# Kernel tuning notes

Hardware: AMD Instinct MI355X
Metric: run time of the kernel (lower is better)

Reference implementation:

```python
import jax, jax.numpy as jnp
import numpy as np

B, C, H, W = 8, 1024, 32, 32   # batch, in_channels (cnn==vit), spatial
OUT = 2048                     # out_channels
NHEAD = 32                     # heads -> head_dim 64
EMBED_DIM = 1024               # used ONLY for the softmax scale (faithful to source)
LN_EPS = 1e-5


def setup_inputs() -> dict:
    key = jax.random.key(0)
    ks = jax.random.split(key, 8)
    f = lambda k, s: jax.random.normal(k, s, dtype=jnp.float32)
    return {
        "x_cnn": f(ks[0], (B, C, H, W)),
        "x_vit": f(ks[1], (B, C, H, W)),
        "Wq": f(ks[2], (OUT, C)) * 0.02, "bq": jnp.zeros((OUT,), jnp.float32),
        "Wk": f(ks[3], (OUT, C)) * 0.02, "bk": jnp.zeros((OUT,), jnp.float32),
        "Wv": f(ks[4], (OUT, C)) * 0.02, "bv": jnp.zeros((OUT,), jnp.float32),
        "w_mix": jnp.float32(0.5),
        "ln_g": jnp.ones((OUT,), jnp.float32), "ln_b": jnp.zeros((OUT,), jnp.float32),
        "Wfc": f(ks[5], (OUT, OUT)) * 0.02, "bfc": jnp.zeros((OUT,), jnp.float32),
    }


def _mha(Q, K, V):
    # Q,K,V: [b, n, OUT] -> multi-head attention, scale by sqrt(EMBED_DIM) as in source
    b, n, _ = Q.shape
    d = OUT // NHEAD
    Qh = Q.reshape(b, n, NHEAD, d)
    Kh = K.reshape(b, n, NHEAD, d)
    Vh = V.reshape(b, n, NHEAD, d)
    scores = jnp.einsum('bqhd,bkhd->bhqk', Qh, Kh) / jnp.sqrt(jnp.float32(EMBED_DIM))
    attn = jax.nn.softmax(scores, axis=-1)
    out = jnp.einsum('bhqk,bkhd->bqhd', attn, Vh)
    return out.reshape(b, n, OUT)


def reference(x_cnn, x_vit, Wq, bq, Wk, bk, Wv, bv, w_mix, ln_g, ln_b, Wfc, bfc):
    b, c, h, w = x_cnn.shape
    xc = x_cnn.reshape(b, c, h * w).transpose(0, 2, 1)   # [b, hw, c]
    xv = x_vit.reshape(b, c, h * w).transpose(0, 2, 1)
    # shared projections, two cross directions
    Q1 = xc @ Wq.T + bq; K1 = xv @ Wk.T + bk; V1 = xv @ Wv.T + bv
    Q2 = xv @ Wq.T + bq; K2 = xc @ Wk.T + bk; V2 = xc @ Wv.T + bv
    attended_vit = _mha(Q1, K1, V1)   # cnn queries attend vit
    attended_cnn = _mha(Q2, K2, V2)   # vit queries attend cnn
    r = attended_cnn * w_mix + attended_vit * (1.0 - w_mix)
    # LayerNorm over last dim (population variance, like torch)
    mu = jnp.mean(r, axis=-1, keepdims=True)
    var = jnp.var(r, axis=-1, keepdims=True)
    r = (r - mu) / jnp.sqrt(var + LN_EPS) * ln_g + ln_b
    r = r @ Wfc.T + bfc
    return r.transpose(0, 2, 1).reshape(b, OUT, h, w)
```

## Files before the change

### kernel.cpp

```cpp
#include <hip/hip_runtime.h>
#include <stdint.h>

typedef unsigned short u16;
typedef unsigned int u32;
typedef __attribute__((ext_vector_type(4))) float float4v;
typedef __attribute__((ext_vector_type(4))) unsigned int uint4v;
typedef __attribute__((ext_vector_type(4))) unsigned short u16x4;
typedef __attribute__((ext_vector_type(8))) short s16x8;
typedef __attribute__((ext_vector_type(4))) float f32x4;

__device__ __forceinline__ float bf2f(u16 h) {
    union { u32 u; float f; } v; v.u = ((u32)h) << 16; return v.f;
}
__device__ __forceinline__ u16 f2bf(float f) {
    union { float f; u32 u; } v; v.f = f;
    return (u16)((v.u + 0x8000u) >> 16);
}
__device__ __forceinline__ float exp2_fast(float x) {
    float r; asm("v_exp_f32 %0, %1" : "=v"(r) : "v"(x)); return r;
}

__device__ __forceinline__ bool detect_f32(const u16* lng) {
    return *(const u32*)lng == 0x3F800000u;
}

__device__ __forceinline__ float read_wmix(const void* wmix) {
    u32 word = *(const u32*)wmix;
    if ((word & 0xFFFFu) == 0u) {
        union { u32 u; float f; } v; v.u = word; return v.f;
    }
    return bf2f((u16)(word & 0xFFFFu));
}

__device__ __forceinline__ uint4v load8(const void* base, long long off, bool isF32) {
    if (isF32) {
        const float* p = (const float*)base + off;
        float4v f0 = *(const float4v*)p;
        float4v f1 = *(const float4v*)(p + 4);
        uint4v r; u16* h = (u16*)&r;
#pragma unroll
        for (int i = 0; i < 4; ++i) { h[i] = f2bf(f0[i]); h[4 + i] = f2bf(f1[i]); }
        return r;
    }
    return *(const uint4v*)((const u16*)base + off);
}
__device__ __forceinline__ float loadraw(const void* p, int idx, bool isF32) {
    return isF32 ? ((const float*)p)[idx] : bf2f(((const u16*)p)[idx]);
}

__global__ __launch_bounds__(256) void convert_w(
    const void* __restrict__ src, u16* __restrict__ dst, int n,
    const u16* __restrict__ lng)
{
    bool f32 = detect_f32(lng);
    long long i = ((long long)blockIdx.x * 256 + threadIdx.x) * 8;
    if (i >= n) return;
    uint4v v = load8(src, i, f32);
    *(uint4v*)(dst + i) = v;
}

__global__ __launch_bounds__(256) void transpose_k(
    const void* __restrict__ xc, const void* __restrict__ xv,
    u16* __restrict__ xt, const u16* __restrict__ lng)
{
    bool f32 = detect_f32(lng);
    int z = blockIdx.z;
    const void* xbase = (z < 8 ? xc : xv);
    long long soff = (long long)(z & 7) * 1024 * 1024;
    u16* outp = xt + (long long)z * 1024 * 1024;
    int c0 = blockIdx.x * 64, p0 = blockIdx.y * 64;
    __shared__ u16 t[64][72];
    int tid = threadIdx.x;
    int cl = tid >> 3, ch = tid & 7;
#pragma unroll
    for (int pass = 0; pass < 2; ++pass) {
        int c = cl + pass * 32;
        uint4v v = load8(xbase, soff + (long long)(c0 + c) * 1024 + p0 + ch * 8, f32);
        const u16* vv = (const u16*)&v;
#pragma unroll
        for (int i = 0; i < 8; ++i) t[ch * 8 + i][c] = vv[i];
    }
    __syncthreads();
#pragma unroll
    for (int pass = 0; pass < 2; ++pass) {
        int p = cl + pass * 32;
        uint4v v; u16* vv = (u16*)&v;
#pragma unroll
        for (int i = 0; i < 8; ++i) vv[i] = t[p][ch * 8 + i];
        *(uint4v*)(outp + (long long)(p0 + p) * 1024 + c0 + ch * 8) = v;
    }
}

__global__ __launch_bounds__(256) void transpose_v(
    const u16* __restrict__ V, u16* __restrict__ VT)
{
    int b = blockIdx.z, head = blockIdx.y, p0 = blockIdx.x * 64;
    const u16* src = V + (long long)b * 1024 * 2048 + head * 64;
    u16* dst = VT + (long long)(b * 32 + head) * 64 * 1024;
    __shared__ u16 t[64][72];
    int tid = threadIdx.x;
    int r = tid >> 3, ch = tid & 7;
#pragma unroll
    for (int pass = 0; pass < 2; ++pass) {
        int p = r + pass * 32;
        uint4v v = *(const uint4v*)(src + (long long)(p0 + p) * 2048 + ch * 8);
        const u16* vv = (const u16*)&v;
#pragma unroll
        for (int i = 0; i < 8; ++i) t[ch * 8 + i][p] = vv[i];
    }
    __syncthreads();
#pragma unroll
    for (int pass = 0; pass < 2; ++pass) {
        int d = r + pass * 32;
        uint4v v = *(const uint4v*)&t[d][ch * 8];
        *(uint4v*)(dst + (long long)d * 1024 + p0 + ch * 8) = v;
    }
}

__global__ __launch_bounds__(256) void gemm_mfma(
    const void* __restrict__ A, int lda, long long sA, int a_raw,
    const void* __restrict__ B, int ldb, long long sB, int b_raw,
    const void* __restrict__ bias,
    void* __restrict__ Cv, int ldc, long long sC, int c_f32,
    int K, int bias_on_m, const u16* __restrict__ lng)
{
    bool f32 = detect_f32(lng);
    bool aF = f32 && a_raw, bF = f32 && b_raw;
    int gx = gridDim.x, gy = gridDim.y, gz = gridDim.z;
    int flat = blockIdx.x + gx * (blockIdx.y + gy * blockIdx.z);
    int nwg = gx * gy * gz;
    int wsw = ((nwg & 7) == 0) ? ((flat & 7) * (nwg >> 3) + (flat >> 3)) : flat;
    int byi = wsw % gy, rem = wsw / gy;
    int bxi = rem % gx, z = rem / gx;

    long long aoff = (long long)z * sA, boff = (long long)z * sB;
    long long coff = (long long)z * sC;
    int m0 = bxi * 128, n0 = byi * 128;
    int tid = threadIdx.x;
    int lane = tid & 63, wave = tid >> 6;
    int lrow = lane & 15, lgrp = lane >> 4;
    int wm = (wave >> 1) * 64, wn = (wave & 1) * 64;

    __shared__ u16 As[128][72];
    __shared__ u16 Bs[128][72];

    f32x4 acc[4][4];
#pragma unroll
    for (int i = 0; i < 4; ++i)
#pragma unroll
        for (int j = 0; j < 4; ++j) acc[i][j] = (f32x4)0.f;

    int sr = tid >> 3;
    int kc = (tid & 7) * 8;

    long long arow[4], brow[4];
#pragma unroll
    for (int q = 0; q < 4; ++q) {
        arow[q] = aoff + (long long)(m0 + sr + q * 32) * lda;
        brow[q] = boff + (long long)(n0 + sr + q * 32) * ldb;
    }

    uint4v an[4], bn[4];
#pragma unroll
    for (int q = 0; q < 4; ++q) {
        an[q] = load8(A, arow[q] + kc, aF);
        bn[q] = load8(B, brow[q] + kc, bF);
    }

    for (int k0 = 0; k0 < K; k0 += 64) {
        uint4v ac[4], bc[4];
#pragma unroll
        for (int q = 0; q < 4; ++q) { ac[q] = an[q]; bc[q] = bn[q]; }
        __syncthreads();
#pragma unroll
        for (int q = 0; q < 4; ++q) {
            *(uint4v*)&As[sr + q * 32][kc] = ac[q];
            *(uint4v*)&Bs[sr + q * 32][kc] = bc[q];
        }
        __syncthreads();
        if (k0 + 64 < K) {
#pragma unroll
            for (int q = 0; q < 4; ++q) {
                an[q] = load8(A, arow[q] + k0 + 64 + kc, aF);
                bn[q] = load8(B, brow[q] + k0 + 64 + kc, bF);
            }
        }
#pragma unroll
        for (int kk = 0; kk < 2; ++kk) {
            s16x8 af[4], bfr[4];
#pragma unroll
            for (int i = 0; i < 4; ++i)
                af[i] = *(const s16x8*)&As[wm + i * 16 + lrow][kk * 32 + lgrp * 8];
#pragma unroll
            for (int j = 0; j < 4; ++j)
                bfr[j] = *(const s16x8*)&Bs[wn + j * 16 + lrow][kk * 32 + lgrp * 8];
#pragma unroll
            for (int i = 0; i < 4; ++i)
#pragma unroll
                for (int j = 0; j < 4; ++j)
                    acc[i][j] = __builtin_amdgcn_mfma_f32_16x16x32_bf16(
                        af[i], bfr[j], acc[i][j], 0, 0, 0);
        }
    }

    float bnj[4];
#pragma unroll
    for (int j = 0; j < 4; ++j)
        bnj[j] = bias_on_m ? 0.f : loadraw(bias, n0 + wn + j * 16 + lrow, f32);
#pragma unroll
    for (int i = 0; i < 4; ++i) {
#pragma unroll
        for (int e = 0; e < 4; ++e) {
            int mrow = m0 + wm + i * 16 + lgrp * 4 + e;
            float bm = bias_on_m ? loadraw(bias, mrow, f32) : 0.f;
#pragma unroll
            for (int j = 0; j < 4; ++j) {
                int ncol = n0 + wn + j * 16 + lrow;
                float val = acc[i][j][e] + (bias_on_m ? bm : bnj[j]);
                long long idx = coff + (long long)mrow * ldc + ncol;
                if (c_f32) ((float*)Cv)[idx] = val;
                else       ((u16*)Cv)[idx] = f2bf(val);
            }
        }
    }
}

__global__ __launch_bounds__(256) void attn_mfma(
    u16* __restrict__ Qb, const u16* __restrict__ Kb, const u16* __restrict__ VTb)
{
    const int ld = 2048;
    const float SCL = 0.0450985123f;
    int flat = blockIdx.x + 16 * (blockIdx.y + 32 * blockIdx.z);
    int w = (flat & 7) * 512 + (flat >> 3);
    int qt = w & 15, head = (w >> 4) & 31, bz = w >> 9;
    int q0 = qt * 64;
    long long base = (long long)bz * 1024 * ld + head * 64;
    u16* Q = Qb + base;
    const u16* K = Kb + base;
    const u16* VT = VTb + (long long)(bz * 32 + head) * 64 * 1024;

    int tid = threadIdx.x;
    int wave = tid >> 6, lane = tid & 63;
    int lrow = lane & 15, lgrp = lane >> 4;

    __shared__ u16 Kt[64][72];
    __shared__ u16 VTt[64][72];
    __shared__ u16 Pt[4][16][72];

    int qw = q0 + wave * 16;
    s16x8 qf0, qf1;
    {
        const u16* qp = Q + (long long)(qw + lrow) * ld + lgrp * 8;
        qf0 = *(const s16x8*)qp;
        qf1 = *(const s16x8*)(qp + 32);
    }
    s16x8 onesf;
#pragma unroll
    for (int e = 0; e < 8; ++e) ((u16*)&onesf)[e] = 0x3F80;

    f32x4 of[4];
#pragma unroll
    for (int dt = 0; dt < 4; ++dt) of[dt] = (f32x4)0.f;
    f32x4 osum = (f32x4)0.f;
    float mL = 0.f;

    int skey = tid >> 2, sc4 = tid & 3;
    const u16* kptr = K + (long long)skey * ld + sc4 * 8;
    const u16* vptr = VT + (long long)skey * 1024 + sc4 * 16;
    uint4v ka0 = *(const uint4v*)kptr;
    uint4v ka1 = *(const uint4v*)(kptr + 32);
    uint4v va0 = *(const uint4v*)vptr;
    uint4v va1 = *(const uint4v*)(vptr + 8);

    for (int t = 0; t < 16; ++t) {
        *(uint4v*)&Kt[skey][sc4 * 8]       = ka0;
        *(uint4v*)&Kt[skey][sc4 * 8 + 32]  = ka1;
        *(uint4v*)&VTt[skey][sc4 * 16]     = va0;
        *(uint4v*)&VTt[skey][sc4 * 16 + 8] = va1;
        if (t < 15) {
            kptr += 64 * ld;
            vptr += 64;
            ka0 = *(const uint4v*)kptr;
            ka1 = *(const uint4v*)(kptr + 32);
            va0 = *(const uint4v*)vptr;
            va1 = *(const uint4v*)(vptr + 8);
        }
        __syncthreads();

        f32x4 sf[4];
#pragma unroll
        for (int f = 0; f < 4; ++f) {
            s16x8 kf0 = *(const s16x8*)&Kt[f * 16 + lrow][lgrp * 8];
            s16x8 kf1 = *(const s16x8*)&Kt[f * 16 + lrow][lgrp * 8 + 32];
            f32x4 a = (f32x4)0.f;
            a = __builtin_amdgcn_mfma_f32_16x16x32_bf16(kf0, qf0, a, 0, 0, 0);
            a = __builtin_amdgcn_mfma_f32_16x16x32_bf16(kf1, qf1, a, 0, 0, 0);
            sf[f] = a;
        }

        float t0 = fmaxf(fmaxf(sf[0][0], sf[0][1]), sf[0][2]);
        float t1 = fmaxf(fmaxf(sf[0][3], sf[1][0]), sf[1][1]);
        float t2 = fmaxf(fmaxf(sf[1][2], sf[1][3]), sf[2][0]);
        float t3 = fmaxf(fmaxf(sf[2][1], sf[2][2]), sf[2][3]);
        float t4 = fmaxf(fmaxf(sf[3][0], sf[3][1]), sf[3][2]);
        float u0 = fmaxf(fmaxf(t0, t1), t2);
        float u1 = fmaxf(fmaxf(t3, t4), sf[3][3]);
        float mx = fmaxf(u0, u1);
        mx = fmaxf(mx, __shfl_xor(mx, 16));
        mx = fmaxf(mx, __shfl_xor(mx, 32));
        if (__any(mx * SCL > mL + 8.f)) {
            float mLn = fmaxf(mL, mx * SCL);
            float sc = exp2_fast(mL - mLn);
#pragma unroll
            for (int dt = 0; dt < 4; ++dt)
#pragma unroll
                for (int i = 0; i < 4; ++i) of[dt][i] *= sc;
#pragma unroll
            for (int i = 0; i < 4; ++i) osum[i] *= sc;
            mL = mLn;
        }

        float nmL = -mL;
#pragma unroll
        for (int f = 0; f < 4; ++f) {
            float p0 = exp2_fast(fmaf(sf[f][0], SCL, nmL));
            float p1 = exp2_fast(fmaf(sf[f][1], SCL, nmL));
            float p2 = exp2_fast(fmaf(sf[f][2], SCL, nmL));
            float p3 = exp2_fast(fmaf(sf[f][3], SCL, nmL));
            union { u32 w[2]; u16x4 v; } pu;
            asm("v_cvt_pk_bf16_f32 %0, %1, %2" : "=v"(pu.w[0]) : "v"(p0), "v"(p1));
            asm("v_cvt_pk_bf16_f32 %0, %1, %2" : "=v"(pu.w[1]) : "v"(p2), "v"(p3));
            *(u16x4*)&Pt[wave][lrow][f * 16 + lgrp * 4] = pu.v;
        }
        asm volatile("s_waitcnt lgkmcnt(0)" ::: "memory");
        __builtin_amdgcn_sched_barrier(0);

#pragma unroll
        for (int kk = 0; kk < 2; ++kk) {
            s16x8 pb = *(const s16x8*)&Pt[wave][lrow][kk * 32 + lgrp * 8];
            osum = __builtin_amdgcn_mfma_f32_16x16x32_bf16(onesf, pb, osum, 0, 0, 0);
#pragma unroll
            for (int dt = 0; dt < 4; ++dt) {
                s16x8 va = *(const s16x8*)&VTt[dt * 16 + lrow][kk * 32 + lgrp * 8];
                of[dt] = __builtin_amdgcn_mfma_f32_16x16x32_bf16(va, pb, of[dt], 0, 0, 0);
            }
        }
        __syncthreads();
    }

    float linv = 1.f / osum[0];
#pragma unroll
    for (int dt = 0; dt < 4; ++dt) {
        u16x4 o;
#pragma unroll
        for (int i = 0; i < 4; ++i) o[i] = f2bf(of[dt][i] * linv);
        *(u16x4*)(Q + (long long)(qw + lrow) * ld + dt * 16 + lgrp * 4) = o;
    }
}

__global__ __launch_bounds__(256) void mix_ln_k(
    const u16* __restrict__ Avit, const u16* __restrict__ Acnn,
    const void* __restrict__ wmix,
    const void* __restrict__ g, const void* __restrict__ bta,
    u16* __restrict__ Y, const u16* __restrict__ lng)
{
    bool f32 = detect_f32(lng);
    long long row = blockIdx.x;
    const u16* a0 = Avit + row * 2048;
    const u16* a1 = Acnn + row * 2048;
    int tid = threadIdx.x, lane = tid & 63, wave = tid >> 6;
    float w = read_wmix(wmix);
    int o = tid * 8;
    uint4v x0 = *(const uint4v*)(a0 + o);
    uint4v x1 = *(const uint4v*)(a1 + o);
    const u16* p0 = (const u16*)&x0;
    const u16* p1 = (const u16*)&x1;
    float r[8], sum = 0.f, sq = 0.f;
#pragma unroll
    for (int e = 0; e < 8; ++e) {
        r[e] = w * bf2f(p1[e]) + (1.f - w) * bf2f(p0[e]);
        sum += r[e]; sq += r[e] * r[e];
    }
#pragma unroll
    for (int off = 1; off < 64; off <<= 1) {
        sum += __shfl_xor(sum, off);
        sq += __shfl_xor(sq, off);
    }
    __shared__ float red[8];
    if (lane == 0) { red[wave] = sum; red[4 + wave] = sq; }
    __syncthreads();
    sum = red[0] + red[1] + red[2] + red[3];
    sq = red[4] + red[5] + red[6] + red[7];
    float mu = sum * (1.f / 2048.f);
    float var = sq * (1.f / 2048.f) - mu * mu;
    float rstd = rsqrtf(var + 1e-5f);
    uint4v y; u16* py = (u16*)&y;
#pragma unroll
    for (int e = 0; e < 8; ++e)
        py[e] = f2bf((r[e] - mu) * rstd * loadraw(g, o + e, f32) + loadraw(bta, o + e, f32));
    *(uint4v*)(Y + row * 2048 + o) = y;
}

extern "C" void kernel_launch(void* const* d_in, const int* in_sizes, int n_in,
                              void* d_out, int out_size, void* d_ws, size_t ws_size,
                              hipStream_t stream)
{
    const void* x_cnn = d_in[0];
    const void* x_vit = d_in[1];
    const void* Wq = d_in[2];
    const void* bq = d_in[3];
    const void* Wk = d_in[4];
    const void* bk = d_in[5];
    const void* Wv = d_in[6];
    const void* bv = d_in[7];
    const void* wmix = d_in[8];
    const u16* ln_g = (const u16*)d_in[9];
    const void* ln_b = d_in[10];
    const void* Wfc = d_in[11];
    const void* bfc = d_in[12];

    u16* X   = (u16*)d_out;
    u16* VTb = (u16*)((char*)d_out + 33554432);
    char* ws = (char*)d_ws;
    const long long SEG = 33554432LL;
    const long long SRC = 8LL * 1024 * 1024;

    bool fused = ws_size >= (size_t)(6 * SEG + 20971520LL);
    bool tail  = fused || ws_size >= (size_t)(4 * SEG + 20971520LL);
    u16* S[6];
    for (int i = 0; i < 6; ++i) S[i] = (u16*)(ws + i * SEG);
    u16* WqB = (u16*)(ws + (fused ? 6 : 4) * SEG);
    u16* WkB = WqB + 2097152;
    u16* WvB = WkB + 2097152;
    u16* WfB = WvB + 2097152;
    if (tail) {
        convert_w<<<1024, 256, 0, stream>>>(Wq, WqB, 2097152, ln_g);
        convert_w<<<1024, 256, 0, stream>>>(Wk, WkB, 2097152, ln_g);
        convert_w<<<1024, 256, 0, stream>>>(Wv, WvB, 2097152, ln_g);
        convert_w<<<2048, 256, 0, stream>>>(Wfc, WfB, 4194304, ln_g);
    }
    const void* pWq = tail ? (const void*)WqB : Wq;
    const void* pWk = tail ? (const void*)WkB : Wk;
    const void* pWv = tail ? (const void*)WvB : Wv;
    const void* pWf = tail ? (const void*)WfB : Wfc;
    int rawW = tail ? 0 : 1;

    transpose_k<<<dim3(16, 16, 16), 256, 0, stream>>>(x_cnn, x_vit, X, ln_g);

    if (fused) {
        dim3 fg(128, 16, 1);
        gemm_mfma<<<fg, 256, 0, stream>>>(X, 1024, 0LL, 0, pWq, 1024, 0LL, rawW, bq,
                                          S[0], 2048, 0LL, 0, 1024, 0, ln_g);
        gemm_mfma<<<fg, 256, 0, stream>>>(X, 1024, 0LL, 0, pWk, 1024, 0LL, rawW, bk,
                                          S[2], 2048, 0LL, 0, 1024, 0, ln_g);
        gemm_mfma<<<fg, 256, 0, stream>>>(X, 1024, 0LL, 0, pWv, 1024, 0LL, rawW, bv,
                                          S[4], 2048, 0LL, 0, 1024, 0, ln_g);
        transpose_v<<<dim3(16, 32, 8), 256, 0, stream>>>(S[5], VTb);
        attn_mfma<<<dim3(16, 32, 8), 256, 0, stream>>>(S[0], S[3], VTb);
        transpose_v<<<dim3(16, 32, 8), 256, 0, stream>>>(S[4], VTb);
        attn_mfma<<<dim3(16, 32, 8), 256, 0, stream>>>(S[1], S[2], VTb);
        mix_ln_k<<<8192, 256, 0, stream>>>(S[0], S[1], wmix, ln_g, ln_b, S[2], ln_g);
    } else {
        dim3 pg(64, 16, 1);
        gemm_mfma<<<pg, 256, 0, stream>>>(X,       1024, 0LL, 0, pWq, 1024, 0LL, rawW, bq,
                                          S[0], 2048, 0LL, 0, 1024, 0, ln_g);
        gemm_mfma<<<pg, 256, 0, stream>>>(X + SRC, 1024, 0LL, 0, pWk, 1024, 0LL, rawW, bk,
                                          S[1], 2048, 0LL, 0, 1024, 0, ln_g);
        gemm_mfma<<<pg, 256, 0, stream>>>(X + SRC, 1024, 0LL, 0, pWv, 1024, 0LL, rawW, bv,
                                          S[2], 2048, 0LL, 0, 1024, 0, ln_g);
        transpose_v<<<dim3(16, 32, 8), 256, 0, stream>>>(S[2], VTb);
        attn_mfma<<<dim3(16, 32, 8), 256, 0, stream>>>(S[0], S[1], VTb);
        gemm_mfma<<<pg, 256, 0, stream>>>(X + SRC, 1024, 0LL, 0, pWq, 1024, 0LL, rawW, bq,
                                          S[1], 2048, 0LL, 0, 1024, 0, ln_g);
        gemm_mfma<<<pg, 256, 0, stream>>>(X,       1024, 0LL, 0, pWk, 1024, 0LL, rawW, bk,
                                          S[2], 2048, 0LL, 0, 1024, 0, ln_g);
        gemm_mfma<<<pg, 256, 0, stream>>>(X,       1024, 0LL, 0, pWv, 1024, 0LL, rawW, bv,
                                          S[3], 2048, 0LL, 0, 1024, 0, ln_g);
        transpose_v<<<dim3(16, 32, 8), 256, 0, stream>>>(S[3], VTb);
        attn_mfma<<<dim3(16, 32, 8), 256, 0, stream>>>(S[1], S[2], VTb);
        mix_ln_k<<<8192, 256, 0, stream>>>(S[0], S[1], wmix, ln_g, ln_b, S[2], ln_g);
    }

    gemm_mfma<<<dim3(16, 8, 8), 256, 0, stream>>>(pWf, 2048, 0LL, rawW, S[2], 2048, 1024LL * 2048, 0, bfc,
                                                  d_out, 1024, 2048LL * 1024, 1, 2048, 1, ln_g);
}
```

Before: 890.5 us.

## Use direct global-to-LDS loads with swizzle in GEMM and merge attention launches

The bf16 GEMM path now loads tiles straight from global memory into LDS with global_load_lds, using an XOR swizzle to avoid bank conflicts. The register staging and software prefetch are dropped, so loads no longer overlap compute within a K step. The two cross-attention directions are merged into one launch with a doubled grid, using separate VT buffers placed in the output region. The online-softmax max reduction is now only done across the full wave when a rescale is needed.

```diff
diff --git a/kernel.cpp b/kernel.cpp
--- a/kernel.cpp
+++ b/kernel.cpp
@@ -18,6 +18,11 @@
 }
 __device__ __forceinline__ float exp2_fast(float x) {
     float r; asm("v_exp_f32 %0, %1" : "=v"(r) : "v"(x)); return r;
+}
+__device__ __forceinline__ void glds16(const u16* g, u16* l) {
+    __builtin_amdgcn_global_load_lds(
+        (const __attribute__((address_space(1))) u32*)(const void*)g,
+        (__attribute__((address_space(3))) u32*)(void*)l, 16, 0, 0);
 }
 
 __device__ __forceinline__ bool detect_f32(const u16* lng) {
@@ -150,56 +155,97 @@
 #pragma unroll
         for (int j = 0; j < 4; ++j) acc[i][j] = (f32x4)0.f;
 
-    int sr = tid >> 3;
-    int kc = (tid & 7) * 8;
-
-    long long arow[4], brow[4];
-#pragma unroll
-    for (int q = 0; q < 4; ++q) {
-        arow[q] = aoff + (long long)(m0 + sr + q * 32) * lda;
-        brow[q] = boff + (long long)(n0 + sr + q * 32) * ldb;
-    }
-
-    uint4v an[4], bn[4];
-#pragma unroll
-    for (int q = 0; q < 4; ++q) {
-        an[q] = load8(A, arow[q] + kc, aF);
-        bn[q] = load8(B, brow[q] + kc, bF);
-    }
-
-    for (int k0 = 0; k0 < K; k0 += 64) {
-        uint4v ac[4], bc[4];
-#pragma unroll
-        for (int q = 0; q < 4; ++q) { ac[q] = an[q]; bc[q] = bn[q]; }
-        __syncthreads();
+    if (!aF && !bF) {
+        u16* Al = (u16*)As;
+        u16* Bl = (u16*)Bs;
+        const u16* Ab = (const u16*)A + aoff;
+        const u16* Bb = (const u16*)B + boff;
+        int rsub = lane >> 3;
+        int csw = ((lane & 7) ^ rsub) * 8;
+        long long ga[4], gb[4];
 #pragma unroll
         for (int q = 0; q < 4; ++q) {
-            *(uint4v*)&As[sr + q * 32][kc] = ac[q];
-            *(uint4v*)&Bs[sr + q * 32][kc] = bc[q];
-        }
-        __syncthreads();
-        if (k0 + 64 < K) {
+            int r = wave * 32 + q * 8 + rsub;
+            ga[q] = (long long)(m0 + r) * lda + csw;
+            gb[q] = (long long)(n0 + r) * ldb + csw;
+        }
+        int xsw = (lrow & 7) * 8;
+        for (int k0 = 0; k0 < K; k0 += 64) {
+            __syncthreads();
 #pragma unroll
             for (int q = 0; q < 4; ++q) {
-                an[q] = load8(A, arow[q] + k0 + 64 + kc, aF);
-                bn[q] = load8(B, brow[q] + k0 + 64 + kc, bF);
-            }
-        }
-#pragma unroll
-        for (int kk = 0; kk < 2; ++kk) {
-            s16x8 af[4], bfr[4];
-#pragma unroll
-            for (int i = 0; i < 4; ++i)
-                af[i] = *(const s16x8*)&As[wm + i * 16 + lrow][kk * 32 + lgrp * 8];
-#pragma unroll
-            for (int j = 0; j < 4; ++j)
-                bfr[j] = *(const s16x8*)&Bs[wn + j * 16 + lrow][kk * 32 + lgrp * 8];
-#pragma unroll
-            for (int i = 0; i < 4; ++i)
+                glds16(Ab + ga[q] + k0, &Al[(wave * 4 + q) * 512]);
+                glds16(Bb + gb[q] + k0, &Bl[(wave * 4 + q) * 512]);
+            }
+            __syncthreads();
+#pragma unroll
+            for (int kk = 0; kk < 2; ++kk) {
+                s16x8 af[4], bfr[4];
+#pragma unroll
+                for (int i = 0; i < 4; ++i)
+                    af[i] = *(const s16x8*)&Al[(wm + i * 16 + lrow) * 64 +
+                                               ((kk * 32 + lgrp * 8) ^ xsw)];
 #pragma unroll
                 for (int j = 0; j < 4; ++j)
-                    acc[i][j] = __builtin_amdgcn_mfma_f32_16x16x32_bf16(
-                        af[i], bfr[j], acc[i][j], 0, 0, 0);
+                    bfr[j] = *(const s16x8*)&Bl[(wn + j * 16 + lrow) * 64 +
+                                                ((kk * 32 + lgrp * 8) ^ xsw)];
+#pragma unroll
+                for (int i = 0; i < 4; ++i)
+#pragma unroll
+                    for (int j = 0; j < 4; ++j)
+                        acc[i][j] = __builtin_amdgcn_mfma_f32_16x16x32_bf16(
+                            af[i], bfr[j], acc[i][j], 0, 0, 0);
+            }
+        }
+    } else {
+        int sr = tid >> 3;
+        int kc = (tid & 7) * 8;
+        long long arow[4], brow[4];
+#pragma unroll
+        for (int q = 0; q < 4; ++q) {
+            arow[q] = aoff + (long long)(m0 + sr + q * 32) * lda;
+            brow[q] = boff + (long long)(n0 + sr + q * 32) * ldb;
+        }
+        uint4v an[4], bn[4];
+#pragma unroll
+        for (int q = 0; q < 4; ++q) {
+            an[q] = load8(A, arow[q] + kc, aF);
+            bn[q] = load8(B, brow[q] + kc, bF);
+        }
+        for (int k0 = 0; k0 < K; k0 += 64) {
+            uint4v ac[4], bc[4];
+#pragma unroll
+            for (int q = 0; q < 4; ++q) { ac[q] = an[q]; bc[q] = bn[q]; }
+            __syncthreads();
+#pragma unroll
+            for (int q = 0; q < 4; ++q) {
+                *(uint4v*)&As[sr + q * 32][kc] = ac[q];
+                *(uint4v*)&Bs[sr + q * 32][kc] = bc[q];
+            }
+            __syncthreads();
+            if (k0 + 64 < K) {
+#pragma unroll
+                for (int q = 0; q < 4; ++q) {
+                    an[q] = load8(A, arow[q] + k0 + 64 + kc, aF);
+                    bn[q] = load8(B, brow[q] + k0 + 64 + kc, bF);
+                }
+            }
+#pragma unroll
+            for (int kk = 0; kk < 2; ++kk) {
+                s16x8 af[4], bfr[4];
+#pragma unroll
+                for (int i = 0; i < 4; ++i)
+                    af[i] = *(const s16x8*)&As[wm + i * 16 + lrow][kk * 32 + lgrp * 8];
+#pragma unroll
+                for (int j = 0; j < 4; ++j)
+                    bfr[j] = *(const s16x8*)&Bs[wn + j * 16 + lrow][kk * 32 + lgrp * 8];
+#pragma unroll
+                for (int i = 0; i < 4; ++i)
+#pragma unroll
+                    for (int j = 0; j < 4; ++j)
+                        acc[i][j] = __builtin_amdgcn_mfma_f32_16x16x32_bf16(
+                            af[i], bfr[j], acc[i][j], 0, 0, 0);
+            }
         }
     }
 
@@ -226,13 +272,19 @@
 }
 
 __global__ __launch_bounds__(256) void attn_mfma(
-    u16* __restrict__ Qb, const u16* __restrict__ Kb, const u16* __restrict__ VTb)
+    u16* __restrict__ Q0b, const u16* __restrict__ K0b, const u16* __restrict__ VT0b,
+    u16* __restrict__ Q1b, const u16* __restrict__ K1b, const u16* __restrict__ VT1b)
 {
     const int ld = 2048;
     const float SCL = 0.0450985123f;
+    int nwg = gridDim.x * gridDim.y * gridDim.z;
     int flat = blockIdx.x + 16 * (blockIdx.y + 32 * blockIdx.z);
-    int w = (flat & 7) * 512 + (flat >> 3);
-    int qt = w & 15, head = (w >> 4) & 31, bz = w >> 9;
+    int w = (flat & 7) * (nwg >> 3) + (flat >> 3);
+    int qt = w & 15, head = (w >> 4) & 31, zz = w >> 9;
+    int bz = zz & 7;
+    u16* Qb; const u16* Kb; const u16* VTb;
+    if (zz < 8) { Qb = Q0b; Kb = K0b; VTb = VT0b; }
+    else        { Qb = Q1b; Kb = K1b; VTb = VT1b; }
     int q0 = qt * 64;
     long long base = (long long)bz * 1024 * ld + head * 64;
     u16* Q = Qb + base;
@@ -305,10 +357,11 @@
         float t4 = fmaxf(fmaxf(sf[3][0], sf[3][1]), sf[3][2]);
         float u0 = fmaxf(fmaxf(t0, t1), t2);
         float u1 = fmaxf(fmaxf(t3, t4), sf[3][3]);
-        float mx = fmaxf(u0, u1);
-        mx = fmaxf(mx, __shfl_xor(mx, 16));
-        mx = fmaxf(mx, __shfl_xor(mx, 32));
-        if (__any(mx * SCL > mL + 8.f)) {
+        float lanemax = fmaxf(u0, u1);
+        if (__any(lanemax * SCL > mL + 8.f)) {
+            float mx = lanemax;
+#pragma unroll
+            for (int off = 1; off < 64; off <<= 1) mx = fmaxf(mx, __shfl_xor(mx, off));
             float mLn = fmaxf(mL, mx * SCL);
             float sc = exp2_fast(mL - mLn);
 #pragma unroll
@@ -420,7 +473,8 @@
     const void* bfc = d_in[12];
 
     u16* X   = (u16*)d_out;
-    u16* VTb = (u16*)((char*)d_out + 33554432);
+    u16* VT0 = (u16*)d_out;
+    u16* VT1 = (u16*)((char*)d_out + 33554432);
     char* ws = (char*)d_ws;
     const long long SEG = 33554432LL;
     const long long SRC = 8LL * 1024 * 1024;
@@ -455,10 +509,10 @@
                                           S[2], 2048, 0LL, 0, 1024, 0, ln_g);
         gemm_mfma<<<fg, 256, 0, stream>>>(X, 1024, 0LL, 0, pWv, 1024, 0LL, rawW, bv,
                                           S[4], 2048, 0LL, 0, 1024, 0, ln_g);
-        transpose_v<<<dim3(16, 32, 8), 256, 0, stream>>>(S[5], VTb);
-        attn_mfma<<<dim3(16, 32, 8), 256, 0, stream>>>(S[0], S[3], VTb);
-        transpose_v<<<dim3(16, 32, 8), 256, 0, stream>>>(S[4], VTb);
-        attn_mfma<<<dim3(16, 32, 8), 256, 0, stream>>>(S[1], S[2], VTb);
+        transpose_v<<<dim3(16, 32, 8), 256, 0, stream>>>(S[5], VT0);
+        transpose_v<<<dim3(16, 32, 8), 256, 0, stream>>>(S[4], VT1);
+        attn_mfma<<<dim3(16, 32, 16), 256, 0, stream>>>(S[0], S[3], VT0,
+                                                        S[1], S[2], VT1);
         mix_ln_k<<<8192, 256, 0, stream>>>(S[0], S[1], wmix, ln_g, ln_b, S[2], ln_g);
     } else {
         dim3 pg(64, 16, 1);
@@ -468,16 +522,18 @@
                                           S[1], 2048, 0LL, 0, 1024, 0, ln_g);
         gemm_mfma<<<pg, 256, 0, stream>>>(X + SRC, 1024, 0LL, 0, pWv, 1024, 0LL, rawW, bv,
                                           S[2], 2048, 0LL, 0, 1024, 0, ln_g);
-        transpose_v<<<dim3(16, 32, 8), 256, 0, stream>>>(S[2], VTb);
-        attn_mfma<<<dim3(16, 32, 8), 256, 0, stream>>>(S[0], S[1], VTb);
+        transpose_v<<<dim3(16, 32, 8), 256, 0, stream>>>(S[2], VT1);
+        attn_mfma<<<dim3(16, 32, 8), 256, 0, stream>>>(S[0], S[1], VT1,
+                                                       S[0], S[1], VT1);
         gemm_mfma<<<pg, 256, 0, stream>>>(X + SRC, 1024, 0LL, 0, pWq, 1024, 0LL, rawW, bq,
                                           S[1], 2048, 0LL, 0, 1024, 0, ln_g);
         gemm_mfma<<<pg, 256, 0, stream>>>(X,       1024, 0LL, 0, pWk, 1024, 0LL, rawW, bk,
                                           S[2], 2048, 0LL, 0, 1024, 0, ln_g);
         gemm_mfma<<<pg, 256, 0, stream>>>(X,       1024, 0LL, 0, pWv, 1024, 0LL, rawW, bv,
                                           S[3], 2048, 0LL, 0, 1024, 0, ln_g);
-        transpose_v<<<dim3(16, 32, 8), 256, 0, stream>>>(S[3], VTb);
-        attn_mfma<<<dim3(16, 32, 8), 256, 0, stream>>>(S[1], S[2], VTb);
+        transpose_v<<<dim3(16, 32, 8), 256, 0, stream>>>(S[3], VT1);
+        attn_mfma<<<dim3(16, 32, 8), 256, 0, stream>>>(S[1], S[2], VT1,
+                                                       S[1], S[2], VT1);
         mix_ln_k<<<8192, 256, 0, stream>>>(S[0], S[1], wmix, ln_g, ln_b, S[2], ln_g);
     }
 
```

After: 882.2 us. About the same (-0.9%).
